# Kernel optimization log

Measured on AMD Instinct MI355X. Metric: run time of the kernel, lower is better.

The kernel has to match this reference:

```python
import jax, jax.numpy as jnp
import numpy as np

N1, N2, D = 8192, 8192, 128

def setup_inputs() -> dict:
    key = jax.random.key(0)
    k1, k2, k3, k4 = jax.random.split(key, 4)
    X1 = jax.random.normal(k1, (N1, D), dtype=jnp.float32)
    X2 = jax.random.normal(k2, (N2, D), dtype=jnp.float32)
    task1 = jax.random.randint(k3, (N1,), 0, 2, dtype=jnp.int32)
    task2 = jax.random.randint(k4, (N2,), 0, 2, dtype=jnp.int32)
    # learned parameters (init values match module defaults: lengthscale=1, output_variance=1, b=0)
    log_l = jnp.zeros((D,), dtype=jnp.float32)          # log(1)
    log_theta_l = jnp.zeros((1,), dtype=jnp.float32)    # log(1)
    b = jnp.zeros((1,), dtype=jnp.float32)
    return {"X1": X1, "X2": X2, "log_l": log_l, "log_theta_l": log_theta_l,
            "b": b, "task1": task1, "task2": task2}

def reference(X1, X2, log_l, log_theta_l, b, task1, task2):
    l = jnp.exp(log_l)                      # (D,) ARD lengthscales
    A = X1 / l                              # (N1, D)
    B = X2 / l                              # (N2, D)
    # sum((a-b)^2) = |a|^2 + |b|^2 - 2 a.b  -> GEMM form, no (N1,N2,D) intermediate
    sq_dist = (jnp.sum(A * A, axis=1)[:, None]
               + jnp.sum(B * B, axis=1)[None, :]
               - 2.0 * (A @ B.T))
    sq_dist = jnp.maximum(sq_dist, 0.0)
    K_base = jnp.exp(log_theta_l[0]) * jnp.exp(-0.5 * sq_dist)   # (N1, N2)
    # lambda = clip(2/(1+exp(b)) - 1, 0, 1)
    lam = jnp.clip(2.0 / (1.0 + jnp.exp(b[0])) - 1.0, 0.0, 1.0)
    diff_task = task1[:, None] != task2[None, :]                 # (N1, N2) bool
    K = K_base * jnp.where(diff_task, lam, 1.0)
    return K
```

## Files before the change

kernel.cpp:

```cpp
#include <hip/hip_runtime.h>
#include <stdint.h>

typedef float f32x4 __attribute__((ext_vector_type(4)));
typedef int   i32x4 __attribute__((ext_vector_type(4)));
typedef __bf16 bf16x8 __attribute__((ext_vector_type(8)));

#define NN 8192
#define DDIM 128

#define APRIME_OFF 0u
#define BPRIME_OFF (8192u*512u)
#define NORM_OFF   (268435456u - 65536u)

__device__ __forceinline__ uint32_t pk2(__bf16 a, __bf16 b) {
    return (uint32_t)__builtin_bit_cast(unsigned short, a)
         | ((uint32_t)__builtin_bit_cast(unsigned short, b) << 16);
}

__device__ __forceinline__ void gload_lds16(const void* g, void* l) {
    __builtin_amdgcn_global_load_lds(
        (const __attribute__((address_space(1))) uint32_t*)g,
        (__attribute__((address_space(3))) uint32_t*)l,
        16, 0, 0);
}

__global__ __launch_bounds__(256) void prep_kernel(
    const float* __restrict__ X1, const float* __restrict__ X2,
    const float* __restrict__ log_l, char* __restrict__ outbuf)
{
    int t = threadIdx.x, wave = t >> 6, lane = t & 63;
    int row = blockIdx.x * 4 + wave;
    const float* X; uint32_t base; float* nrm;
    if (row < NN) {
        X = X1 + (size_t)row * DDIM;
        base = APRIME_OFF + (uint32_t)row * 512u;
        nrm = (float*)(outbuf + NORM_OFF) + row;
    } else {
        int r2 = row - NN;
        X = X2 + (size_t)r2 * DDIM;
        base = BPRIME_OFF + (uint32_t)r2 * 512u;
        nrm = (float*)(outbuf + NORM_OFF) + NN + r2;
    }
    int c0 = lane * 2;
    float2 x = *(const float2*)(X + c0);
    float a0 = x.x * __expf(-log_l[c0]);
    float a1 = x.y * __expf(-log_l[c0 + 1]);
    float ss = a0 * a0 + a1 * a1;
    #pragma unroll
    for (int o = 32; o; o >>= 1) ss += __shfl_down(ss, o);
    if (lane == 0) *nrm = ss;
    __bf16 h0 = (__bf16)a0, h1 = (__bf16)a1;
    __bf16 l0 = (__bf16)(a0 - (float)h0), l1 = (__bf16)(a1 - (float)h1);
    int m = lane >> 2;
    int c = m >> 2;
    int sh = m & 3;
    int sl = 4 | sh;
    int rs = row & 7;
    uint32_t offh = base + (uint32_t)c * 128u + (uint32_t)((sh ^ rs) * 16) + (uint32_t)(lane & 3) * 4u;
    uint32_t offl = base + (uint32_t)c * 128u + (uint32_t)((sl ^ rs) * 16) + (uint32_t)(lane & 3) * 4u;
    *(uint32_t*)(outbuf + offh) = pk2(h0, h1);
    *(uint32_t*)(outbuf + offl) = pk2(l0, l1);
}

__global__ __launch_bounds__(256, 2) void fast_kernel(
    const char* __restrict__ stash,
    const int* __restrict__ task1, const int* __restrict__ task2,
    const float* __restrict__ log_theta_l, const float* __restrict__ bparam,
    float* __restrict__ C)
{
    __shared__ __align__(16) char smem[65536];
    const int t = threadIdx.x;
    const int lane = t & 63, wv = t >> 6;
    const int lr = lane & 15, lg = lane >> 4;
    const float* n1g = (const float*)(stash + NORM_OFF);
    const float* n2g = n1g + NN;
    float logt = log_theta_l[0];
    float bb = bparam[0];
    float lam = fminf(fmaxf(2.f / (1.f + __expf(bb)) - 1.f, 0.f), 1.f);
    int wg = blockIdx.x;

    if (wg < 3840) {
        const int wr = wv >> 1, wc = wv & 1;
        int swz = (wg & 7) * 480 + (wg >> 3);
        int tm = 2 + (swz >> 6);
        int tn = swz & 63;
        const char* Abase = stash + APRIME_OFF + (size_t)tm * 128 * 512;
        const char* Bbase = stash + BPRIME_OFF + (size_t)tn * 128 * 512;

        f32x4 acc[4][4];
        #pragma unroll
        for (int i = 0; i < 4; ++i)
            #pragma unroll
            for (int j = 0; j < 4; ++j) acc[i][j] = (f32x4){0.f, 0.f, 0.f, 0.f};

        #define STAGE_F(c, buf) do {                                              \
            _Pragma("unroll")                                                     \
            for (int i = 0; i < 4; ++i) {                                         \
                int l = t + i * 256;                                              \
                gload_lds16(Abase + (size_t)(l >> 3) * 512 + (c) * 128 + (l & 7) * 16,\
                            smem + (buf) * 32768 + l * 16);                       \
                gload_lds16(Bbase + (size_t)(l >> 3) * 512 + (c) * 128 + (l & 7) * 16,\
                            smem + (buf) * 32768 + 16384 + l * 16);               \
            }                                                                     \
        } while (0)

        #define FRAGMM_F(buf) do {                                                \
            const char* tb_ = smem + (buf) * 32768;                               \
            bf16x8 ah[4], bh[4], xf[4];                                           \
            _Pragma("unroll")                                                     \
            for (int mi = 0; mi < 4; ++mi) {                                      \
                int row = wr * 64 + mi * 16 + lr;                                 \
                ah[mi] = *(const bf16x8*)(tb_ + row * 128 + ((lg ^ (row & 7)) * 16));\
            }                                                                     \
            _Pragma("unroll")                                                     \
            for (int ni = 0; ni < 4; ++ni) {                                      \
                int row = wc * 64 + ni * 16 + lr;                                 \
                bh[ni] = *(const bf16x8*)(tb_ + 16384 + row * 128                 \
                          + ((lg ^ (row & 7)) * 16));                             \
            }                                                                     \
            _Pragma("unroll")                                                     \
            for (int mi = 0; mi < 4; ++mi)                                        \
                _Pragma("unroll")                                                 \
                for (int ni = 0; ni < 4; ++ni)                                    \
                    acc[mi][ni] = __builtin_amdgcn_mfma_f32_16x16x32_bf16(        \
                        bh[ni], ah[mi], acc[mi][ni], 0, 0, 0);                    \
            _Pragma("unroll")                                                     \
            for (int mi = 0; mi < 4; ++mi) {                                      \
                int row = wr * 64 + mi * 16 + lr;                                 \
                xf[mi] = *(const bf16x8*)(tb_ + row * 128                         \
                          + (((4 | lg) ^ (row & 7)) * 16));                       \
            }                                                                     \
            _Pragma("unroll")                                                     \
            for (int mi = 0; mi < 4; ++mi)                                        \
                _Pragma("unroll")                                                 \
                for (int ni = 0; ni < 4; ++ni)                                    \
                    acc[mi][ni] = __builtin_amdgcn_mfma_f32_16x16x32_bf16(        \
                        bh[ni], xf[mi], acc[mi][ni], 0, 0, 0);                    \
            _Pragma("unroll")                                                     \
            for (int ni = 0; ni < 4; ++ni) {                                      \
                int row = wc * 64 + ni * 16 + lr;                                 \
                xf[ni] = *(const bf16x8*)(tb_ + 16384 + row * 128                 \
                          + (((4 | lg) ^ (row & 7)) * 16));                       \
            }                                                                     \
            _Pragma("unroll")                                                     \
            for (int mi = 0; mi < 4; ++mi)                                        \
                _Pragma("unroll")                                                 \
                for (int ni = 0; ni < 4; ++ni)                                    \
                    acc[mi][ni] = __builtin_amdgcn_mfma_f32_16x16x32_bf16(        \
                        xf[ni], ah[mi], acc[mi][ni], 0, 0, 0);                    \
        } while (0)

        STAGE_F(0, 0);
        __syncthreads();
        STAGE_F(1, 1);  FRAGMM_F(0);  __syncthreads();
        STAGE_F(2, 0);  FRAGMM_F(1);  __syncthreads();
        STAGE_F(3, 1);  FRAGMM_F(0);  __syncthreads();
                        FRAGMM_F(1);

        int rbase = tm * 128, cbase = tn * 128;
        #pragma unroll
        for (int mi = 0; mi < 4; ++mi) {
            int rowl = wr * 64 + mi * 16 + lr;
            float n1v = n1g[rbase + rowl];
            int t1v = task1[rbase + rowl];
            #pragma unroll
            for (int ni = 0; ni < 4; ++ni) {
                int coll = wc * 64 + ni * 16 + lg * 4;
                f32x4 n2v = *(const f32x4*)(n2g + cbase + coll);
                i32x4 t2v = *(const i32x4*)(task2 + cbase + coll);
                f32x4 kv;
                #pragma unroll
                for (int rix = 0; rix < 4; ++rix) {
                    float s = fmaxf(n1v + n2v[rix] - 2.f * acc[mi][ni][rix], 0.f);
                    float k = __expf(fmaf(-0.5f, s, logt));
                    kv[rix] = (t1v != t2v[rix]) ? k * lam : k;
                }
                __builtin_nontemporal_store(kv,
                    (f32x4*)(C + (size_t)(rbase + rowl) * NN + cbase + coll));
            }
        }
        #undef STAGE_F
        #undef FRAGMM_F
    } else {
        int wq = wg - 3840;
        int tn = wq >> 2;
        int q = wq & 3;
        int arow0 = 62 * 128 + (q >> 1) * 64;
        int brow0 = tn * 128 + (q & 1) * 64;
        const int wr = wv >> 1, wc = wv & 1;
        const char* Abase = stash + APRIME_OFF + (size_t)arow0 * 512;
        const char* Bbase = stash + BPRIME_OFF + (size_t)brow0 * 512;

        f32x4 acc[2][2];
        #pragma unroll
        for (int i = 0; i < 2; ++i)
            #pragma unroll
            for (int j = 0; j < 2; ++j) acc[i][j] = (f32x4){0.f, 0.f, 0.f, 0.f};

        #define STAGE_Q(c, buf) do {                                              \
            _Pragma("unroll")                                                     \
            for (int i = 0; i < 2; ++i) {                                         \
                int l = t + i * 256;                                              \
                gload_lds16(Abase + (size_t)(l >> 3) * 512 + (c) * 128 + (l & 7) * 16,\
                            smem + (buf) * 32768 + l * 16);                       \
                gload_lds16(Bbase + (size_t)(l >> 3) * 512 + (c) * 128 + (l & 7) * 16,\
                            smem + (buf) * 32768 + 8192 + l * 16);               \
            }                                                                     \
        } while (0)

        #define FRAGMM_Q(buf) do {                                                \
            const char* tb_ = smem + (buf) * 32768;                               \
            bf16x8 ah[2], bh[2], xf[2];                                           \
            _Pragma("unroll")                                                     \
            for (int mi = 0; mi < 2; ++mi) {                                      \
                int row = wr * 32 + mi * 16 + lr;                                 \
                ah[mi] = *(const bf16x8*)(tb_ + row * 128 + ((lg ^ (row & 7)) * 16));\
            }                                                                     \
            _Pragma("unroll")                                                     \
            for (int ni = 0; ni < 2; ++ni) {                                      \
                int row = wc * 32 + ni * 16 + lr;                                 \
                bh[ni] = *(const bf16x8*)(tb_ + 8192 + row * 128                  \
                          + ((lg ^ (row & 7)) * 16));                             \
            }                                                                     \
            _Pragma("unroll")                                                     \
            for (int mi = 0; mi < 2; ++mi)                                        \
                _Pragma("unroll")                                                 \
                for (int ni = 0; ni < 2; ++ni)                                    \
                    acc[mi][ni] = __builtin_amdgcn_mfma_f32_16x16x32_bf16(        \
                        bh[ni], ah[mi], acc[mi][ni], 0, 0, 0);                    \
            _Pragma("unroll")                                                     \
            for (int mi = 0; mi < 2; ++mi) {                                      \
                int row = wr * 32 + mi * 16 + lr;                                 \
                xf[mi] = *(const bf16x8*)(tb_ + row * 128                         \
                          + (((4 | lg) ^ (row & 7)) * 16));                       \
            }                                                                     \
            _Pragma("unroll")                                                     \
            for (int mi = 0; mi < 2; ++mi)                                        \
                _Pragma("unroll")                                                 \
                for (int ni = 0; ni < 2; ++ni)                                    \
                    acc[mi][ni] = __builtin_amdgcn_mfma_f32_16x16x32_bf16(        \
                        bh[ni], xf[mi], acc[mi][ni], 0, 0, 0);                    \
            _Pragma("unroll")                                                     \
            for (int ni = 0; ni < 2; ++ni) {                                      \
                int row = wc * 32 + ni * 16 + lr;                                 \
                xf[ni] = *(const bf16x8*)(tb_ + 8192 + row * 128                  \
                          + (((4 | lg) ^ (row & 7)) * 16));                       \
            }                                                                     \
            _Pragma("unroll")                                                     \
            for (int mi = 0; mi < 2; ++mi)                                        \
                _Pragma("unroll")                                                 \
                for (int ni = 0; ni < 2; ++ni)                                    \
                    acc[mi][ni] = __builtin_amdgcn_mfma_f32_16x16x32_bf16(        \
                        xf[ni], ah[mi], acc[mi][ni], 0, 0, 0);                    \
        } while (0)

        STAGE_Q(0, 0);
        __syncthreads();
        STAGE_Q(1, 1);  FRAGMM_Q(0);  __syncthreads();
        STAGE_Q(2, 0);  FRAGMM_Q(1);  __syncthreads();
        STAGE_Q(3, 1);  FRAGMM_Q(0);  __syncthreads();
                        FRAGMM_Q(1);

        #pragma unroll
        for (int mi = 0; mi < 2; ++mi) {
            int rowl = wr * 32 + mi * 16 + lr;
            float n1v = n1g[arow0 + rowl];
            int t1v = task1[arow0 + rowl];
            #pragma unroll
            for (int ni = 0; ni < 2; ++ni) {
                int coll = wc * 32 + ni * 16 + lg * 4;
                f32x4 n2v = *(const f32x4*)(n2g + brow0 + coll);
                i32x4 t2v = *(const i32x4*)(task2 + brow0 + coll);
                f32x4 kv;
                #pragma unroll
                for (int rix = 0; rix < 4; ++rix) {
                    float s = fmaxf(n1v + n2v[rix] - 2.f * acc[mi][ni][rix], 0.f);
                    float k = __expf(fmaf(-0.5f, s, logt));
                    kv[rix] = (t1v != t2v[rix]) ? k * lam : k;
                }
                __builtin_nontemporal_store(kv,
                    (f32x4*)(C + (size_t)(arow0 + rowl) * NN + brow0 + coll));
            }
        }
        #undef STAGE_Q
        #undef FRAGMM_Q
    }
}

#define RSTRIDE 80
#define SQ_AH 0
#define SQ_AL 5120
#define SQ_BH 10240
#define SQ_BL 15360
#define SQ_ILS 20480
#define SQ_N1  20992
#define SQ_N2  21504
#define SQ_TOT 22016

__device__ __forceinline__ void split4(f32x4 x, uint2& hi, uint2& lo) {
    __bf16 h0 = (__bf16)x[0], h1 = (__bf16)x[1], h2 = (__bf16)x[2], h3 = (__bf16)x[3];
    hi.x = pk2(h0, h1); hi.y = pk2(h2, h3);
    __bf16 l0 = (__bf16)(x[0] - (float)h0);
    __bf16 l1 = (__bf16)(x[1] - (float)h1);
    __bf16 l2 = (__bf16)(x[2] - (float)h2);
    __bf16 l3 = (__bf16)(x[3] - (float)h3);
    lo.x = pk2(l0, l1); lo.y = pk2(l2, l3);
}

__device__ __forceinline__ void lds_barrier() {
    asm volatile("s_waitcnt lgkmcnt(0)" ::: "memory");
    __builtin_amdgcn_sched_barrier(0);
    __builtin_amdgcn_s_barrier();
    __builtin_amdgcn_sched_barrier(0);
}

__global__ __launch_bounds__(256, 3) void slow_kernel(
    const float* __restrict__ X1, const float* __restrict__ X2,
    const float* __restrict__ log_l,
    const float* __restrict__ log_theta_l, const float* __restrict__ bparam,
    const int* __restrict__ task1, const int* __restrict__ task2,
    float* __restrict__ C)
{
    __shared__ __align__(16) char smem[SQ_TOT];
    float* const ils = (float*)(smem + SQ_ILS);
    float* const n1s = (float*)(smem + SQ_N1);
    float* const n2s = (float*)(smem + SQ_N2);

    const int t = threadIdx.x;
    const int lane = t & 63;
    const int wv = t >> 6;
    const int wr = wv >> 1, wc = wv & 1;
    const int lr = lane & 15, lg = lane >> 4;
    const int kq = t & 7;
    const int rg = t >> 3;

    int wg = blockIdx.x;
    int ti = wg >> 2;
    int tsel = ti >> 6;
    int tm = (tsel == 2) ? 63 : tsel;
    int tn = ti & 63;
    int q = wg & 3;
    int row0 = tm * 128 + (q >> 1) * 64;
    int col0 = tn * 128 + (q & 1) * 64;

    const float* Ag = X1 + (size_t)row0 * DDIM;
    const float* Bg = X2 + (size_t)col0 * DDIM;

    if (t < 128) ils[t] = __expf(-log_l[t]);

    f32x4 aV[2], bV[2];
    #pragma unroll
    for (int e = 0; e < 2; ++e) {
        aV[e] = *(const f32x4*)(Ag + (size_t)(e * 32 + rg) * DDIM + kq * 4);
        bV[e] = *(const f32x4*)(Bg + (size_t)(e * 32 + rg) * DDIM + kq * 4);
    }
    __syncthreads();

    float nA[2] = {0.f, 0.f};
    float nB[2] = {0.f, 0.f};
    f32x4 acc[2][2];
    #pragma unroll
    for (int i = 0; i < 2; ++i)
        #pragma unroll
        for (int j = 0; j < 2; ++j) acc[i][j] = (f32x4){0.f, 0.f, 0.f, 0.f};

    for (int c = 0; c < 4; ++c) {
        {
            f32x4 il4 = *(const f32x4*)(ils + c * 32 + kq * 4);
            #pragma unroll
            for (int e = 0; e < 2; ++e) {
                int rr = e * 32 + rg;
                f32x4 xa = aV[e] * il4;
                f32x4 xb = bV[e] * il4;
                nA[e] += xa[0]*xa[0] + xa[1]*xa[1] + xa[2]*xa[2] + xa[3]*xa[3];
                nB[e] += xb[0]*xb[0] + xb[1]*xb[1] + xb[2]*xb[2] + xb[3]*xb[3];
                uint2 hA, lA, hB, lB;
                split4(xa, hA, lA);
                split4(xb, hB, lB);
                int boff = rr * RSTRIDE + kq * 8;
                *(uint2*)(smem + SQ_AH + boff) = hA;
                *(uint2*)(smem + SQ_AL + boff) = lA;
                *(uint2*)(smem + SQ_BH + boff) = hB;
                *(uint2*)(smem + SQ_BL + boff) = lB;
            }
        }
        if (c < 3) {
            #pragma unroll
            for (int e = 0; e < 2; ++e) {
                aV[e] = *(const f32x4*)(Ag + (size_t)(e * 32 + rg) * DDIM + (c + 1) * 32 + kq * 4);
                bV[e] = *(const f32x4*)(Bg + (size_t)(e * 32 + rg) * DDIM + (c + 1) * 32 + kq * 4);
            }
        }
        lds_barrier();
        {
            bf16x8 ah[2], bh[2], xf[2];
            #pragma unroll
            for (int mi = 0; mi < 2; ++mi) {
                int off = (wr * 32 + mi * 16 + lr) * RSTRIDE + lg * 16;
                ah[mi] = *(const bf16x8*)(smem + SQ_AH + off);
            }
            #pragma unroll
            for (int ni = 0; ni < 2; ++ni) {
                int off = (wc * 32 + ni * 16 + lr) * RSTRIDE + lg * 16;
                bh[ni] = *(const bf16x8*)(smem + SQ_BH + off);
            }
            #pragma unroll
            for (int mi = 0; mi < 2; ++mi)
                #pragma unroll
                for (int ni = 0; ni < 2; ++ni)
                    acc[mi][ni] = __builtin_amdgcn_mfma_f32_16x16x32_bf16(bh[ni], ah[mi], acc[mi][ni], 0, 0, 0);
            #pragma unroll
            for (int mi = 0; mi < 2; ++mi) {
                int off = (wr * 32 + mi * 16 + lr) * RSTRIDE + lg * 16;
                xf[mi] = *(const bf16x8*)(smem + SQ_AL + off);
            }
            #pragma unroll
            for (int mi = 0; mi < 2; ++mi)
                #pragma unroll
                for (int ni = 0; ni < 2; ++ni)
                    acc[mi][ni] = __builtin_amdgcn_mfma_f32_16x16x32_bf16(bh[ni], xf[mi], acc[mi][ni], 0, 0, 0);
            #pragma unroll
            for (int ni = 0; ni < 2; ++ni) {
                int off = (wc * 32 + ni * 16 + lr) * RSTRIDE + lg * 16;
                xf[ni] = *(const bf16x8*)(smem + SQ_BL + off);
            }
            #pragma unroll
            for (int mi = 0; mi < 2; ++mi)
                #pragma unroll
                for (int ni = 0; ni < 2; ++ni)
                    acc[mi][ni] = __builtin_amdgcn_mfma_f32_16x16x32_bf16(xf[ni], ah[mi], acc[mi][ni], 0, 0, 0);
        }
        lds_barrier();
    }

    #pragma unroll
    for (int e = 0; e < 2; ++e) {
        #pragma unroll
        for (int off = 1; off < 8; off <<= 1) {
            nA[e] += __shfl_xor(nA[e], off);
            nB[e] += __shfl_xor(nB[e], off);
        }
    }
    if (kq == 0) {
        #pragma unroll
        for (int e = 0; e < 2; ++e) {
            n1s[e * 32 + rg] = nA[e];
            n2s[e * 32 + rg] = nB[e];
        }
    }
    __syncthreads();

    float logt = log_theta_l[0];
    float bb = bparam[0];
    float lam = fminf(fmaxf(2.f / (1.f + __expf(bb)) - 1.f, 0.f), 1.f);

    #pragma unroll
    for (int mi = 0; mi < 2; ++mi) {
        int rowl = wr * 32 + mi * 16 + lr;
        float n1v = n1s[rowl];
        int t1v = task1[row0 + rowl];
        #pragma unroll
        for (int ni = 0; ni < 2; ++ni) {
            int coll = wc * 32 + ni * 16 + lg * 4;
            f32x4 n2v = *(const f32x4*)(n2s + coll);
            i32x4 t2v = *(const i32x4*)(task2 + col0 + coll);
            f32x4 kv;
            #pragma unroll
            for (int rix = 0; rix < 4; ++rix) {
                float s = fmaxf(n1v + n2v[rix] - 2.f * acc[mi][ni][rix], 0.f);
                float k = __expf(fmaf(-0.5f, s, logt));
                kv[rix] = (t1v != t2v[rix]) ? k * lam : k;
            }
            *(f32x4*)(C + (size_t)(row0 + rowl) * NN + col0 + coll) = kv;
        }
    }
}

extern "C" void kernel_launch(void* const* d_in, const int* in_sizes, int n_in,
                              void* d_out, int out_size, void* d_ws, size_t ws_size,
                              hipStream_t stream)
{
    const float* X1 = (const float*)d_in[0];
    const float* X2 = (const float*)d_in[1];
    const float* log_l = (const float*)d_in[2];
    const float* log_theta = (const float*)d_in[3];
    const float* bp = (const float*)d_in[4];
    const int* t1 = (const int*)d_in[5];
    const int* t2 = (const int*)d_in[6];
    float* C = (float*)d_out;
    (void)d_ws; (void)ws_size; (void)in_sizes; (void)n_in; (void)out_size;

    prep_kernel<<<4096, 256, 0, stream>>>(X1, X2, log_l, (char*)d_out);
    fast_kernel<<<4096, 256, 0, stream>>>((const char*)d_out, t1, t2, log_theta, bp, C);
    slow_kernel<<<768, 256, 0, stream>>>(X1, X2, log_l, log_theta, bp, t1, t2, C);
}
```

Before: 99.43 us.

## Use explicit vmcnt/lgkmcnt waits to keep next stage loads in flight; batch prep rows

Replaces __syncthreads in the double-buffered GEMM pipelines with explicit s_waitcnt vmcnt(N) plus s_barrier. The next stage's global-to-LDS loads can then stay in flight while the current buffer is consumed, instead of draining all memory ops at every barrier. The prep kernel also now processes 4 rows per wave with a quarter of the blocks, which cuts launch and block overhead. Hand-counted vmcnt values carry a correctness risk if the compiler emits other memory ops, and the sched_barriers constrain instruction scheduling.

```diff
diff --git a/kernel.cpp b/kernel.cpp
--- a/kernel.cpp
+++ b/kernel.cpp
@@ -24,42 +24,59 @@
         16, 0, 0);
 }
 
+#define BAR_VMCNT(N) do {                                          \
+    asm volatile("s_waitcnt vmcnt(" #N ")" ::: "memory");          \
+    __builtin_amdgcn_sched_barrier(0);                             \
+    __builtin_amdgcn_s_barrier();                                  \
+    __builtin_amdgcn_sched_barrier(0);                             \
+} while (0)
+
+#define BAR_LGKM() do {                                            \
+    asm volatile("s_waitcnt lgkmcnt(0)" ::: "memory");             \
+    __builtin_amdgcn_sched_barrier(0);                             \
+    __builtin_amdgcn_s_barrier();                                  \
+    __builtin_amdgcn_sched_barrier(0);                             \
+} while (0)
+
 __global__ __launch_bounds__(256) void prep_kernel(
     const float* __restrict__ X1, const float* __restrict__ X2,
     const float* __restrict__ log_l, char* __restrict__ outbuf)
 {
     int t = threadIdx.x, wave = t >> 6, lane = t & 63;
-    int row = blockIdx.x * 4 + wave;
-    const float* X; uint32_t base; float* nrm;
-    if (row < NN) {
-        X = X1 + (size_t)row * DDIM;
-        base = APRIME_OFF + (uint32_t)row * 512u;
-        nrm = (float*)(outbuf + NORM_OFF) + row;
-    } else {
-        int r2 = row - NN;
-        X = X2 + (size_t)r2 * DDIM;
-        base = BPRIME_OFF + (uint32_t)r2 * 512u;
-        nrm = (float*)(outbuf + NORM_OFF) + NN + r2;
-    }
     int c0 = lane * 2;
-    float2 x = *(const float2*)(X + c0);
-    float a0 = x.x * __expf(-log_l[c0]);
-    float a1 = x.y * __expf(-log_l[c0 + 1]);
-    float ss = a0 * a0 + a1 * a1;
     #pragma unroll
-    for (int o = 32; o; o >>= 1) ss += __shfl_down(ss, o);
-    if (lane == 0) *nrm = ss;
-    __bf16 h0 = (__bf16)a0, h1 = (__bf16)a1;
-    __bf16 l0 = (__bf16)(a0 - (float)h0), l1 = (__bf16)(a1 - (float)h1);
-    int m = lane >> 2;
-    int c = m >> 2;
-    int sh = m & 3;
-    int sl = 4 | sh;
-    int rs = row & 7;
-    uint32_t offh = base + (uint32_t)c * 128u + (uint32_t)((sh ^ rs) * 16) + (uint32_t)(lane & 3) * 4u;
-    uint32_t offl = base + (uint32_t)c * 128u + (uint32_t)((sl ^ rs) * 16) + (uint32_t)(lane & 3) * 4u;
-    *(uint32_t*)(outbuf + offh) = pk2(h0, h1);
-    *(uint32_t*)(outbuf + offl) = pk2(l0, l1);
+    for (int i = 0; i < 4; ++i) {
+        int row = blockIdx.x * 16 + wave * 4 + i;
+        const float* X; uint32_t base; float* nrm;
+        if (row < NN) {
+            X = X1 + (size_t)row * DDIM;
+            base = APRIME_OFF + (uint32_t)row * 512u;
+            nrm = (float*)(outbuf + NORM_OFF) + row;
+        } else {
+            int r2 = row - NN;
+            X = X2 + (size_t)r2 * DDIM;
+            base = BPRIME_OFF + (uint32_t)r2 * 512u;
+            nrm = (float*)(outbuf + NORM_OFF) + NN + r2;
+        }
+        float2 x = *(const float2*)(X + c0);
+        float a0 = x.x * __expf(-log_l[c0]);
+        float a1 = x.y * __expf(-log_l[c0 + 1]);
+        float ss = a0 * a0 + a1 * a1;
+        #pragma unroll
+        for (int o = 32; o; o >>= 1) ss += __shfl_down(ss, o);
+        if (lane == 0) *nrm = ss;
+        __bf16 h0 = (__bf16)a0, h1 = (__bf16)a1;
+        __bf16 l0 = (__bf16)(a0 - (float)h0), l1 = (__bf16)(a1 - (float)h1);
+        int m = lane >> 2;
+        int c = m >> 2;
+        int sh = m & 3;
+        int sl = 4 | sh;
+        int rs = row & 7;
+        uint32_t offh = base + (uint32_t)c * 128u + (uint32_t)((sh ^ rs) * 16) + (uint32_t)(lane & 3) * 4u;
+        uint32_t offl = base + (uint32_t)c * 128u + (uint32_t)((sl ^ rs) * 16) + (uint32_t)(lane & 3) * 4u;
+        *(uint32_t*)(outbuf + offh) = pk2(h0, h1);
+        *(uint32_t*)(outbuf + offl) = pk2(l0, l1);
+    }
 }
 
 __global__ __launch_bounds__(256, 2) void fast_kernel(
@@ -151,11 +168,19 @@
         } while (0)
 
         STAGE_F(0, 0);
-        __syncthreads();
-        STAGE_F(1, 1);  FRAGMM_F(0);  __syncthreads();
-        STAGE_F(2, 0);  FRAGMM_F(1);  __syncthreads();
-        STAGE_F(3, 1);  FRAGMM_F(0);  __syncthreads();
-                        FRAGMM_F(1);
+        STAGE_F(1, 1);
+        BAR_VMCNT(8);
+        FRAGMM_F(0);
+        BAR_LGKM();
+        STAGE_F(2, 0);
+        BAR_VMCNT(8);
+        FRAGMM_F(1);
+        BAR_LGKM();
+        STAGE_F(3, 1);
+        BAR_VMCNT(8);
+        FRAGMM_F(0);
+        BAR_VMCNT(0);
+        FRAGMM_F(1);
 
         int rbase = tm * 128, cbase = tn * 128;
         #pragma unroll
@@ -204,7 +229,7 @@
                 gload_lds16(Abase + (size_t)(l >> 3) * 512 + (c) * 128 + (l & 7) * 16,\
                             smem + (buf) * 32768 + l * 16);                       \
                 gload_lds16(Bbase + (size_t)(l >> 3) * 512 + (c) * 128 + (l & 7) * 16,\
-                            smem + (buf) * 32768 + 8192 + l * 16);               \
+                            smem + (buf) * 32768 + 8192 + l * 16);                \
             }                                                                     \
         } while (0)
 
@@ -255,11 +280,19 @@
         } while (0)
 
         STAGE_Q(0, 0);
-        __syncthreads();
-        STAGE_Q(1, 1);  FRAGMM_Q(0);  __syncthreads();
-        STAGE_Q(2, 0);  FRAGMM_Q(1);  __syncthreads();
-        STAGE_Q(3, 1);  FRAGMM_Q(0);  __syncthreads();
-                        FRAGMM_Q(1);
+        STAGE_Q(1, 1);
+        BAR_VMCNT(4);
+        FRAGMM_Q(0);
+        BAR_LGKM();
+        STAGE_Q(2, 0);
+        BAR_VMCNT(4);
+        FRAGMM_Q(1);
+        BAR_LGKM();
+        STAGE_Q(3, 1);
+        BAR_VMCNT(4);
+        FRAGMM_Q(0);
+        BAR_VMCNT(0);
+        FRAGMM_Q(1);
 
         #pragma unroll
         for (int mi = 0; mi < 2; ++mi) {
@@ -490,7 +523,7 @@
     float* C = (float*)d_out;
     (void)d_ws; (void)ws_size; (void)in_sizes; (void)n_in; (void)out_size;
 
-    prep_kernel<<<4096, 256, 0, stream>>>(X1, X2, log_l, (char*)d_out);
+    prep_kernel<<<1024, 256, 0, stream>>>(X1, X2, log_l, (char*)d_out);
     fast_kernel<<<4096, 256, 0, stream>>>((const char*)d_out, t1, t2, log_theta, bp, C);
     slow_kernel<<<768, 256, 0, stream>>>(X1, X2, log_l, log_theta, bp, t1, t2, C);
 }
```

After: 97.37 us. 2.1% less time.
